# Kernel tuning notes

Hardware: AMD Instinct MI355X
Metric: run time of the kernel (lower is better)

Reference implementation:

```python
import jax, jax.numpy as jnp
from jax import lax
import numpy as np

PN_FEAT = 64


def _conv(x, w, b):
    # x: [B,H,W,Cin], w: [kh,kw,Cin,Cout] (SAME padding, stride 1)
    return lax.conv_general_dilated(x, w, (1, 1), 'SAME',
                                    dimension_numbers=('NHWC', 'HWIO', 'NHWC')) + b


def setup_inputs() -> dict:
    key = jax.random.key(0)
    ks = jax.random.split(key, 12)
    B, P, N, C = 4, 5000, 100, 8
    nx = ny = 240
    pillars = jax.random.normal(ks[0], (B, P, N, C), dtype=jnp.float32)
    pillar_idxs = jax.random.randint(ks[1], (B, P, 2), 0, nx).astype(jnp.int32)
    def lin(k, fi, fo):
        return jax.random.normal(k, (fi, fo), dtype=jnp.float32) / np.sqrt(fi).astype(np.float32)
    def cnv(k, kh, kw, ci, co):
        return jax.random.normal(k, (kh, kw, ci, co), dtype=jnp.float32) / np.sqrt(kh * kw * ci).astype(np.float32)
    return {
        'pillars': pillars,
        'pillar_idxs': pillar_idxs,
        'nx': nx,
        'ny': ny,
        # pointnet MLP: 8 -> 64 (tanh) -> 64
        'pn_w0': lin(ks[2], 8, 64), 'pn_b0': jnp.zeros((64,), jnp.float32),
        'pn_w1': lin(ks[3], 64, PN_FEAT), 'pn_b1': jnp.zeros((PN_FEAT,), jnp.float32),
        # resnet costmap CNN: 64 -> 128 (tanh) -> 128 (tanh) -> 1, relu output
        'cw0': cnv(ks[4], 3, 3, PN_FEAT, 128), 'cb0': jnp.zeros((128,), jnp.float32),
        'cw1': cnv(ks[5], 3, 3, 128, 128), 'cb1': jnp.zeros((128,), jnp.float32),
        'cw2': cnv(ks[6], 1, 1, 128, 1), 'cb2': jnp.zeros((1,), jnp.float32),
    }


def reference(pillars, pillar_idxs, nx, ny,
              pn_w0, pn_b0, pn_w1, pn_b1,
              cw0, cb0, cw1, cb1, cw2, cb2):
    VALID_THRESH = 1000000.0
    ACT_SCALE = 1.0
    # mask padded points (norm >= 1e6 means invalid)
    valid = (jnp.linalg.norm(pillars, axis=-1, keepdims=True) < VALID_THRESH).astype(pillars.dtype)
    # per-point MLP: [B,P,N,8] -> [B,P,N,F]
    h = jnp.tanh(pillars @ pn_w0 + pn_b0)
    feat = h @ pn_w1 + pn_b1
    # masked max over points in each pillar -> [B,P,F]
    pmax = jnp.max(feat * valid, axis=-2)
    # scatter pillar features into BEV pseudo-image [B,nx,ny,F]
    B = pillars.shape[0]
    bidx = jnp.arange(B)[:, None]                      # [B,1]
    img = jnp.zeros((B, nx, ny, PN_FEAT), pillars.dtype)
    img = img.at[bidx, pillar_idxs[..., 0], pillar_idxs[..., 1]].set(pmax)
    # costmap CNN head (NHWC internally; original is NCHW, same math)
    x = jnp.tanh(_conv(img, cw0, cb0))
    x = jnp.tanh(_conv(x, cw1, cb1))
    x = _conv(x, cw2, cb2)
    return jax.nn.relu(x) * ACT_SCALE            # [B,nx,ny,1]
```

## Files before the change

kernel.cpp:

```cpp
#include <hip/hip_runtime.h>
#include <hip/hip_bf16.h>
#include <math.h>

#define B  4
#define P  5000
#define NPT 100
#define F  64
#define NX 240
#define NY 240
#define C1 128

typedef __attribute__((ext_vector_type(8)))  short short8;
typedef __attribute__((ext_vector_type(16))) float f32x16;

__device__ __forceinline__ float tanh_fast(float x) {
    float e = __expf(2.0f * x);
    float r = __builtin_amdgcn_rcpf(e + 1.0f);
    return __builtin_fmaf(-2.0f, r, 1.0f);
}
__device__ __forceinline__ short bf16_bits(float f) {
    return (short)(__bfloat16_as_ushort(__float2bfloat16(f)));
}

__global__ __launch_bounds__(128) void pn_mfma_kernel(
    const float* __restrict__ pillars,
    const short* __restrict__ w0p,
    const float* __restrict__ b0,
    const __hip_bfloat16* __restrict__ w1t,
    const float* __restrict__ b1,
    float* __restrict__ pmax)
{
    constexpr int HS = F + 8;
    constexpr int XS = 40;
    __shared__ short xA[128 * XS];
    __shared__ short hA[128 * HS];
    __shared__ float red[2][F];
    __shared__ unsigned int vb32[4];

    int bp = blockIdx.x;
    int n  = threadIdx.x;
    int wave = n >> 6, lane = n & 63;
    int mr = lane & 31;
    int g  = lane >> 5;
    bool live = (n < NPT);

    const float* xp = pillars + ((size_t)bp * NPT + (live ? n : 0)) * 8;
    float4 q0 = *(const float4*)xp;
    float4 q1 = *(const float4*)(xp + 4);
    float x[8] = {q0.x, q0.y, q0.z, q0.w, q1.x, q1.y, q1.z, q1.w};

    float ss = 0.f;
#pragma unroll
    for (int c = 0; c < 8; c++) ss += x[c] * x[c];
    bool valid = live && (ss < 1e12f);

    unsigned long long bal = __ballot(valid);
    if (lane == 0) {
        vb32[wave * 2]     = (unsigned)bal;
        vb32[wave * 2 + 1] = (unsigned)(bal >> 32);
    }

    short8 xhi, xlo, xz;
#pragma unroll
    for (int c = 0; c < 8; c++) {
        __hip_bfloat16 hb = __float2bfloat16(x[c]);
        float hv = __bfloat162float(hb);
        xhi[c] = (short)__bfloat16_as_ushort(hb);
        xlo[c] = bf16_bits(x[c] - hv);
        xz[c] = 0;
    }
    *(short8*)&xA[n * XS + 0]  = xhi;
    *(short8*)&xA[n * XS + 8]  = xlo;
    *(short8*)&xA[n * XS + 16] = xhi;
    *(short8*)&xA[n * XS + 24] = xz;
    __syncthreads();

    short8 wb[2][2];
#pragma unroll
    for (int kk = 0; kk < 2; kk++)
#pragma unroll
        for (int nt = 0; nt < 2; nt++)
            wb[kk][nt] = *(const short8*)(w0p + ((kk * 2 + g) * 64 + nt * 32 + mr) * 8);

    f32x16 hc00 = {0,0,0,0,0,0,0,0,0,0,0,0,0,0,0,0};
    f32x16 hc01 = hc00, hc10 = hc00, hc11 = hc00;
#pragma unroll
    for (int kk = 0; kk < 2; kk++) {
        short8 a0 = *(const short8*)&xA[(wave * 64 + mr) * XS + kk * 16 + g * 8];
        short8 a1 = *(const short8*)&xA[(wave * 64 + 32 + mr) * XS + kk * 16 + g * 8];
        hc00 = __builtin_amdgcn_mfma_f32_32x32x16_bf16(a0, wb[kk][0], hc00, 0, 0, 0);
        hc01 = __builtin_amdgcn_mfma_f32_32x32x16_bf16(a0, wb[kk][1], hc01, 0, 0, 0);
        hc10 = __builtin_amdgcn_mfma_f32_32x32x16_bf16(a1, wb[kk][0], hc10, 0, 0, 0);
        hc11 = __builtin_amdgcn_mfma_f32_32x32x16_bf16(a1, wb[kk][1], hc11, 0, 0, 0);
    }

    float b00 = b0[mr];
    float b01 = b0[32 + mr];
#pragma unroll
    for (int mt = 0; mt < 2; mt++) {
#pragma unroll
        for (int r = 0; r < 16; r++) {
            int prow = wave * 64 + mt * 32 + (r & 3) + 8 * (r >> 2) + 4 * g;
            float h0 = (mt == 0) ? hc00[r] : hc10[r];
            float h1 = (mt == 0) ? hc01[r] : hc11[r];
            hA[prow * HS + mr]      = bf16_bits(tanh_fast(h0 + b00));
            hA[prow * HS + 32 + mr] = bf16_bits(tanh_fast(h1 + b01));
        }
    }
    __syncthreads();

    short8 bfrag[2][4];
#pragma unroll
    for (int nt = 0; nt < 2; nt++)
#pragma unroll
        for (int c0 = 0; c0 < 4; c0++)
            bfrag[nt][c0] = *(const short8*)((const short*)w1t +
                                (nt * 32 + mr) * F + c0 * 16 + g * 8);

    f32x16 acc00 = {0,0,0,0,0,0,0,0,0,0,0,0,0,0,0,0};
    f32x16 acc01 = acc00, acc10 = acc00, acc11 = acc00;

    const short* arow = &hA[(wave * 64 + mr) * HS + g * 8];
#pragma unroll
    for (int c0 = 0; c0 < 4; c0++) {
        short8 af0 = *(const short8*)(arow + c0 * 16);
        short8 af1 = *(const short8*)(arow + 32 * HS + c0 * 16);
        acc00 = __builtin_amdgcn_mfma_f32_32x32x16_bf16(af0, bfrag[0][c0], acc00, 0, 0, 0);
        acc01 = __builtin_amdgcn_mfma_f32_32x32x16_bf16(af0, bfrag[1][c0], acc01, 0, 0, 0);
        acc10 = __builtin_amdgcn_mfma_f32_32x32x16_bf16(af1, bfrag[0][c0], acc10, 0, 0, 0);
        acc11 = __builtin_amdgcn_mfma_f32_32x32x16_bf16(af1, bfrag[1][c0], acc11, 0, 0, 0);
    }

    float bv0 = b1[mr];
    float bv1 = b1[32 + mr];
    bool allv = ((vb32[0] & vb32[1] & vb32[2]) == 0xFFFFFFFFu) &&
                ((vb32[3] & 0xFu) == 0xFu);
    float mx0 = -INFINITY, mx1 = -INFINITY;

    if (allv) {
#pragma unroll
        for (int mt = 0; mt < 2; mt++) {
#pragma unroll
            for (int r = 0; r < 16; r++) {
                bool inc = !(wave == 1 && mt == 1) || (g == 0 && r < 4);
                if (inc) {
                    mx0 = fmaxf(mx0, (mt == 0) ? acc00[r] : acc10[r]);
                    mx1 = fmaxf(mx1, (mt == 0) ? acc01[r] : acc11[r]);
                }
            }
        }
        mx0 += bv0;
        mx1 += bv1;
    } else {
        unsigned wm0 = vb32[wave * 2];
        unsigned wm1 = vb32[wave * 2 + 1];
#pragma unroll
        for (int mt = 0; mt < 2; mt++) {
            unsigned wm = (mt == 0) ? wm0 : wm1;
#pragma unroll
            for (int r = 0; r < 16; r++) {
                int idx = (r & 3) + 8 * (r >> 2) + 4 * g;
                bool inc = !(wave == 1 && mt == 1) || (idx < 4);
                if (inc) {
                    bool vbit = (wm >> idx) & 1;
                    float a0 = (mt == 0) ? acc00[r] : acc10[r];
                    float a1 = (mt == 0) ? acc01[r] : acc11[r];
                    mx0 = fmaxf(mx0, vbit ? (a0 + bv0) : 0.0f);
                    mx1 = fmaxf(mx1, vbit ? (a1 + bv1) : 0.0f);
                }
            }
        }
    }
    mx0 = fmaxf(mx0, __shfl_xor(mx0, 32, 64));
    mx1 = fmaxf(mx1, __shfl_xor(mx1, 32, 64));
    if (lane < 32) { red[wave][mr] = mx0; red[wave][32 + mr] = mx1; }
    __syncthreads();
    if (n < F)
        pmax[(size_t)bp * F + n] = fmaxf(red[0][n], red[1][n]);
}

__global__ __launch_bounds__(256) void winner_kernel(
    const int* __restrict__ idxs, int* __restrict__ winner)
{
    int i = blockIdx.x * 256 + threadIdx.x;
    if (i >= B * P) return;
    int ix = idxs[i * 2], iy = idxs[i * 2 + 1];
    int b = i / P, p = i % P;
    atomicMax(&winner[(b * NX + ix) * NY + iy], p);
}

__global__ __launch_bounds__(64) void scatter_kernel(
    const int* __restrict__ idxs, const int* __restrict__ winner,
    const float* __restrict__ pmax, __hip_bfloat16* __restrict__ img)
{
    int bp = blockIdx.x;
    int f = threadIdx.x;
    int ix = idxs[bp * 2], iy = idxs[bp * 2 + 1];
    int b = bp / P, p = bp % P;
    int cell = (b * NX + ix) * NY + iy;
    if (winner[cell] == p)
        img[(size_t)cell * F + f] = __float2bfloat16(pmax[(size_t)bp * F + f]);
}

__global__ __launch_bounds__(256) void cvt_w_kernel(
    const float* __restrict__ w, __hip_bfloat16* __restrict__ wt, int cin)
{
    int idx = blockIdx.x * 256 + threadIdx.x;
    int total = 9 * cin * 128;
    if (idx >= total) return;
    int co = idx % 128;
    int rest = idx / 128;
    int ci = rest % cin;
    int t  = rest / cin;
    int c0 = ci >> 4, c16 = ci & 15;
    wt[(((size_t)(t * (cin >> 4) + c0)) * 128 + co) * 16 + c16] = __float2bfloat16(w[idx]);
}

__global__ __launch_bounds__(256) void cvt_w1_kernel(
    const float* __restrict__ w1, __hip_bfloat16* __restrict__ w1t)
{
    int idx = blockIdx.x * 256 + threadIdx.x;
    if (idx >= F * F) return;
    int k = idx >> 6, nn = idx & 63;
    w1t[nn * F + k] = __float2bfloat16(w1[idx]);
}

__global__ __launch_bounds__(256) void cvt_w0p_kernel(
    const float* __restrict__ w0, short* __restrict__ w0p)
{
    int idx = blockIdx.x * 256 + threadIdx.x;
    if (idx >= 4 * 64 * 8) return;
    int j = idx & 7;
    int nn = (idx >> 3) & 63;
    int s = idx >> 9;
    float wv = w0[j * F + nn];
    __hip_bfloat16 hb = __float2bfloat16(wv);
    short out = 0;
    if (s < 2)      out = (short)__bfloat16_as_ushort(hb);
    else if (s == 2) out = bf16_bits(wv - __bfloat162float(hb));
    w0p[idx] = out;
}

template<int CIN, bool FUSE>
__global__ __launch_bounds__(256, 3) void conv_mfma(
    const __hip_bfloat16* __restrict__ in,
    const __hip_bfloat16* __restrict__ wt,
    const float* __restrict__ bias,
    const float* __restrict__ w2,
    const float* __restrict__ b2,
    __hip_bfloat16* __restrict__ out_bf,
    float* __restrict__ out_f)
{
    constexpr int PASSES = CIN / 64;
    constexpr int CI   = 64;
    constexpr int NC16 = CI / 16;
    constexpr int ROWS = 4 * 98;
    __shared__ short sP[ROWS * 64];
    __shared__ float sred[FUSE ? 2 : 1][2][96];

    int tid  = threadIdx.x;
    int wave = tid >> 6;
    int lane = tid & 63;
    int mr = lane & 31;
    int g  = lane >> 5;
    int coh = wave & 1;
    int xr  = wave >> 1;
    int x0 = blockIdx.x * 2;
    int y0 = blockIdx.y * 72;
    int b  = blockIdx.z;
    int n0 = coh * 64;

    const short* wts = (const short*)wt;

    f32x16 acc[3][2];
#pragma unroll
    for (int mt = 0; mt < 3; mt++)
#pragma unroll
        for (int nt = 0; nt < 2; nt++)
            acc[mt][nt] = (f32x16){0,0,0,0,0,0,0,0,0,0,0,0,0,0,0,0};

#pragma unroll
    for (int p = 0; p < PASSES; p++) {
        if (p) __syncthreads();

        for (int i = 0; i < 13; i++) {
            int t = tid + i * 256;
            if (t < ROWS * 8) {
                int c8  = t & 7;
                int row = t >> 3;
                int dx = row / 98, dy = row - dx * 98;
                int gx = x0 - 1 + dx, gy = y0 - 1 + dy;
                float4 v = make_float4(0.f, 0.f, 0.f, 0.f);
                if (gx >= 0 && gx < NX && gy >= 0 && gy < NY)
                    v = *(const float4*)&in[(((size_t)b * NX + gx) * NY + gy) * CIN + p * CI + c8 * 8];
                *(float4*)&sP[row * 64 + ((c8 ^ (row & 7)) * 8)] = v;
            }
        }
        __syncthreads();

#pragma unroll
        for (int tap = 0; tap < 9; tap++) {
            int kh = tap / 3, kw = tap % 3;
            int rowbase = (xr + kh) * 98 + kw + mr;
            int r7 = rowbase & 7;
            const short* abase = sP + rowbase * 64;
            const short* wrow = wts + ((size_t)(tap * (CIN / 16) + p * NC16) * 128 + n0 + mr) * 16 + g * 8;
#pragma unroll
            for (int c0 = 0; c0 < NC16; c0++) {
                short8 w0f = *(const short8*)(wrow + (size_t)c0 * 2048);
                short8 w1f = *(const short8*)(wrow + (size_t)c0 * 2048 + 512);
                int goff = ((c0 * 2 + g) ^ r7) * 8;
                short8 a0 = *(const short8*)(abase + goff);
                short8 a1 = *(const short8*)(abase + 32 * 64 + goff);
                short8 a2 = *(const short8*)(abase + 64 * 64 + goff);
                acc[0][0] = __builtin_amdgcn_mfma_f32_32x32x16_bf16(a0, w0f, acc[0][0], 0, 0, 0);
                acc[0][1] = __builtin_amdgcn_mfma_f32_32x32x16_bf16(a0, w1f, acc[0][1], 0, 0, 0);
                acc[1][0] = __builtin_amdgcn_mfma_f32_32x32x16_bf16(a1, w0f, acc[1][0], 0, 0, 0);
                acc[1][1] = __builtin_amdgcn_mfma_f32_32x32x16_bf16(a1, w1f, acc[1][1], 0, 0, 0);
                acc[2][0] = __builtin_amdgcn_mfma_f32_32x32x16_bf16(a2, w0f, acc[2][0], 0, 0, 0);
                acc[2][1] = __builtin_amdgcn_mfma_f32_32x32x16_bf16(a2, w1f, acc[2][1], 0, 0, 0);
            }
        }
    }

    float bv0 = bias[n0 + mr];
    float bv1 = bias[n0 + 32 + mr];
    if (!FUSE) {
        size_t base = ((size_t)b * NX + (x0 + xr)) * NY;
#pragma unroll
        for (int mt = 0; mt < 3; mt++) {
#pragma unroll
            for (int r = 0; r < 16; r++) {
                int y = y0 + mt * 32 + (r & 3) + 8 * (r >> 2) + 4 * g;
                out_bf[(base + y) * C1 + n0 + mr]      = __float2bfloat16(tanh_fast(acc[mt][0][r] + bv0));
                out_bf[(base + y) * C1 + n0 + 32 + mr] = __float2bfloat16(tanh_fast(acc[mt][1][r] + bv1));
            }
        }
    } else {
        float w20 = w2[n0 + mr];
        float w21 = w2[n0 + 32 + mr];
#pragma unroll
        for (int mt = 0; mt < 3; mt++) {
#pragma unroll
            for (int r = 0; r < 16; r++) {
                float v = tanh_fast(acc[mt][0][r] + bv0) * w20
                        + tanh_fast(acc[mt][1][r] + bv1) * w21;
                v += __shfl_xor(v, 1, 64);
                v += __shfl_xor(v, 2, 64);
                v += __shfl_xor(v, 4, 64);
                v += __shfl_xor(v, 8, 64);
                v += __shfl_xor(v, 16, 64);
                if (mr == 0)
                    sred[coh][xr][mt * 32 + (r & 3) + 8 * (r >> 2) + 4 * g] = v;
            }
        }
        __syncthreads();
        if (tid < 192) {
            int xr2 = tid / 96;
            int yy  = tid % 96;
            float r = sred[0][xr2][yy] + sred[1][xr2][yy] + b2[0];
            out_f[((size_t)b * NX + (x0 + xr2)) * NY + (y0 + yy)] = fmaxf(r, 0.f);
        }
    }
}

extern "C" void kernel_launch(void* const* d_in, const int* in_sizes, int n_in,
                              void* d_out, int out_size, void* d_ws, size_t ws_size,
                              hipStream_t stream) {
    const float* pillars = (const float*)d_in[0];
    const int*   idxs    = (const int*)d_in[1];
    const float* pn_w0   = (const float*)d_in[4];
    const float* pn_b0   = (const float*)d_in[5];
    const float* pn_w1   = (const float*)d_in[6];
    const float* pn_b1   = (const float*)d_in[7];
    const float* cw0     = (const float*)d_in[8];
    const float* cb0     = (const float*)d_in[9];
    const float* cw1     = (const float*)d_in[10];
    const float* cb1     = (const float*)d_in[11];
    const float* cw2     = (const float*)d_in[12];
    const float* cb2     = (const float*)d_in[13];
    float* out = (float*)d_out;

    char* ws = (char*)d_ws;
    const size_t IMG_BYTES  = (size_t)B * NX * NY * F * 2;
    const size_t OUT1_BYTES = (size_t)B * NX * NY * C1 * 2;
    const size_t WIN_BYTES  = (size_t)B * NX * NY * 4;
    const size_t PMAX_BYTES = (size_t)B * P * F * 4;
    const size_t WT1_BYTES  = (size_t)9 * C1 * F * 2;
    const size_t WT2_BYTES  = (size_t)9 * C1 * C1 * 2;
    const size_t W1T_BYTES  = (size_t)F * F * 2;
    __hip_bfloat16* img  = (__hip_bfloat16*)ws;
    __hip_bfloat16* out1 = (__hip_bfloat16*)(ws + IMG_BYTES);
    int*   winner = (int*)(ws + IMG_BYTES + OUT1_BYTES);
    float* pmax   = (float*)(ws + IMG_BYTES + OUT1_BYTES + WIN_BYTES);
    __hip_bfloat16* wt1 = (__hip_bfloat16*)(ws + IMG_BYTES + OUT1_BYTES + WIN_BYTES + PMAX_BYTES);
    __hip_bfloat16* wt2 = (__hip_bfloat16*)(ws + IMG_BYTES + OUT1_BYTES + WIN_BYTES + PMAX_BYTES + WT1_BYTES);
    __hip_bfloat16* w1t = (__hip_bfloat16*)(ws + IMG_BYTES + OUT1_BYTES + WIN_BYTES + PMAX_BYTES + WT1_BYTES + WT2_BYTES);
    short* w0p = (short*)(ws + IMG_BYTES + OUT1_BYTES + WIN_BYTES + PMAX_BYTES + WT1_BYTES + WT2_BYTES + W1T_BYTES);

    hipMemsetAsync(img, 0, IMG_BYTES, stream);
    hipMemsetAsync(winner, 0xFF, WIN_BYTES, stream);

    cvt_w_kernel<<<(9 * F * C1 + 255) / 256, 256, 0, stream>>>(cw0, wt1, F);
    cvt_w_kernel<<<(9 * C1 * C1 + 255) / 256, 256, 0, stream>>>(cw1, wt2, C1);
    cvt_w1_kernel<<<(F * F + 255) / 256, 256, 0, stream>>>(pn_w1, w1t);
    cvt_w0p_kernel<<<(4 * 64 * 8 + 255) / 256, 256, 0, stream>>>(pn_w0, w0p);

    pn_mfma_kernel<<<B * P, 128, 0, stream>>>(pillars, w0p, pn_b0, w1t, pn_b1, pmax);
    winner_kernel<<<(B * P + 255) / 256, 256, 0, stream>>>(idxs, winner);
    scatter_kernel<<<B * P, 64, 0, stream>>>(idxs, winner, pmax, img);

    conv_mfma<F, false><<<dim3(NX / 2, 3, B), 256, 0, stream>>>(
        img, wt1, cb0, nullptr, nullptr, out1, nullptr);
    conv_mfma<C1, true><<<dim3(NX / 2, 3, B), 256, 0, stream>>>(
        out1, wt2, cb1, cw2, cb2, nullptr, out);
}
```

Baseline: 386.7 us.

## Stage conv input tiles with async global-to-LDS loads and smaller row tiles

```diff
diff --git a/kernel.cpp b/kernel.cpp
--- a/kernel.cpp
+++ b/kernel.cpp
@@ -20,6 +20,11 @@
 }
 __device__ __forceinline__ short bf16_bits(float f) {
     return (short)(__bfloat16_as_ushort(__float2bfloat16(f)));
+}
+__device__ __forceinline__ void async_load16(const void* g, void* l) {
+    __builtin_amdgcn_global_load_lds(
+        (const __attribute__((address_space(1))) void*)g,
+        (__attribute__((address_space(3))) void*)l, 16, 0, 0);
 }
 
 __global__ __launch_bounds__(128) void pn_mfma_kernel(
@@ -248,15 +253,16 @@
     const float* __restrict__ bias,
     const float* __restrict__ w2,
     const float* __restrict__ b2,
+    const __hip_bfloat16* __restrict__ zerobuf,
     __hip_bfloat16* __restrict__ out_bf,
     float* __restrict__ out_f)
 {
     constexpr int PASSES = CIN / 64;
     constexpr int CI   = 64;
     constexpr int NC16 = CI / 16;
-    constexpr int ROWS = 4 * 98;
-    __shared__ short sP[ROWS * 64];
-    __shared__ float sred[FUSE ? 2 : 1][2][96];
+    constexpr int CSTR = 272;
+    __shared__ short sP[8 * CSTR * 8];
+    __shared__ float sred[FUSE ? 2 : 1][2][64];
 
     int tid  = threadIdx.x;
     int wave = tid >> 6;
@@ -266,15 +272,16 @@
     int coh = wave & 1;
     int xr  = wave >> 1;
     int x0 = blockIdx.x * 2;
-    int y0 = blockIdx.y * 72;
+    int y0 = blockIdx.y * 62;
+    if (y0 > 178) y0 = 178;
     int b  = blockIdx.z;
     int n0 = coh * 64;
 
     const short* wts = (const short*)wt;
 
-    f32x16 acc[3][2];
-#pragma unroll
-    for (int mt = 0; mt < 3; mt++)
+    f32x16 acc[2][2];
+#pragma unroll
+    for (int mt = 0; mt < 2; mt++)
 #pragma unroll
         for (int nt = 0; nt < 2; nt++)
             acc[mt][nt] = (f32x16){0,0,0,0,0,0,0,0,0,0,0,0,0,0,0,0};
@@ -283,17 +290,20 @@
     for (int p = 0; p < PASSES; p++) {
         if (p) __syncthreads();
 
-        for (int i = 0; i < 13; i++) {
-            int t = tid + i * 256;
-            if (t < ROWS * 8) {
-                int c8  = t & 7;
-                int row = t >> 3;
-                int dx = row / 98, dy = row - dx * 98;
-                int gx = x0 - 1 + dx, gy = y0 - 1 + dy;
-                float4 v = make_float4(0.f, 0.f, 0.f, 0.f);
-                if (gx >= 0 && gx < NX && gy >= 0 && gy < NY)
-                    v = *(const float4*)&in[(((size_t)b * NX + gx) * NY + gy) * CIN + p * CI + c8 * 8];
-                *(float4*)&sP[row * 64 + ((c8 ^ (row & 7)) * 8)] = v;
+        {
+            int gy = y0 - 1 + lane;
+            bool yok = (gy >= 0 && gy < NY);
+#pragma unroll
+            for (int j = 0; j < 8; j++) {
+                int q  = j * 4 + wave;
+                int cc = q >> 2;
+                int dx = q & 3;
+                int gx = x0 - 1 + dx;
+                const __hip_bfloat16* src =
+                    (yok && gx >= 0 && gx < NX)
+                    ? &in[(((size_t)b * NX + gx) * NY + gy) * CIN + p * CI + cc * 8]
+                    : zerobuf;
+                async_load16(src, (void*)(sP + (cc * CSTR + dx * 64) * 8));
             }
         }
         __syncthreads();
@@ -301,24 +311,20 @@
 #pragma unroll
         for (int tap = 0; tap < 9; tap++) {
             int kh = tap / 3, kw = tap % 3;
-            int rowbase = (xr + kh) * 98 + kw + mr;
-            int r7 = rowbase & 7;
-            const short* abase = sP + rowbase * 64;
+            int rowcol = (xr + kh) * 64 + kw;
             const short* wrow = wts + ((size_t)(tap * (CIN / 16) + p * NC16) * 128 + n0 + mr) * 16 + g * 8;
 #pragma unroll
             for (int c0 = 0; c0 < NC16; c0++) {
                 short8 w0f = *(const short8*)(wrow + (size_t)c0 * 2048);
                 short8 w1f = *(const short8*)(wrow + (size_t)c0 * 2048 + 512);
-                int goff = ((c0 * 2 + g) ^ r7) * 8;
-                short8 a0 = *(const short8*)(abase + goff);
-                short8 a1 = *(const short8*)(abase + 32 * 64 + goff);
-                short8 a2 = *(const short8*)(abase + 64 * 64 + goff);
+                int cc = c0 * 2 + g;
+                const short* abase = sP + (cc * CSTR + rowcol + mr) * 8;
+                short8 a0 = *(const short8*)(abase);
+                short8 a1 = *(const short8*)(abase + 32 * 8);
                 acc[0][0] = __builtin_amdgcn_mfma_f32_32x32x16_bf16(a0, w0f, acc[0][0], 0, 0, 0);
                 acc[0][1] = __builtin_amdgcn_mfma_f32_32x32x16_bf16(a0, w1f, acc[0][1], 0, 0, 0);
                 acc[1][0] = __builtin_amdgcn_mfma_f32_32x32x16_bf16(a1, w0f, acc[1][0], 0, 0, 0);
                 acc[1][1] = __builtin_amdgcn_mfma_f32_32x32x16_bf16(a1, w1f, acc[1][1], 0, 0, 0);
-                acc[2][0] = __builtin_amdgcn_mfma_f32_32x32x16_bf16(a2, w0f, acc[2][0], 0, 0, 0);
-                acc[2][1] = __builtin_amdgcn_mfma_f32_32x32x16_bf16(a2, w1f, acc[2][1], 0, 0, 0);
             }
         }
     }
@@ -328,19 +334,22 @@
     if (!FUSE) {
         size_t base = ((size_t)b * NX + (x0 + xr)) * NY;
 #pragma unroll
-        for (int mt = 0; mt < 3; mt++) {
+        for (int mt = 0; mt < 2; mt++) {
 #pragma unroll
             for (int r = 0; r < 16; r++) {
-                int y = y0 + mt * 32 + (r & 3) + 8 * (r >> 2) + 4 * g;
-                out_bf[(base + y) * C1 + n0 + mr]      = __float2bfloat16(tanh_fast(acc[mt][0][r] + bv0));
-                out_bf[(base + y) * C1 + n0 + 32 + mr] = __float2bfloat16(tanh_fast(acc[mt][1][r] + bv1));
+                int row = mt * 32 + (r & 3) + 8 * (r >> 2) + 4 * g;
+                if (row < 62) {
+                    int y = y0 + row;
+                    out_bf[(base + y) * C1 + n0 + mr]      = __float2bfloat16(tanh_fast(acc[mt][0][r] + bv0));
+                    out_bf[(base + y) * C1 + n0 + 32 + mr] = __float2bfloat16(tanh_fast(acc[mt][1][r] + bv1));
+                }
             }
         }
     } else {
         float w20 = w2[n0 + mr];
         float w21 = w2[n0 + 32 + mr];
 #pragma unroll
-        for (int mt = 0; mt < 3; mt++) {
+        for (int mt = 0; mt < 2; mt++) {
 #pragma unroll
             for (int r = 0; r < 16; r++) {
                 float v = tanh_fast(acc[mt][0][r] + bv0) * w20
@@ -355,11 +364,13 @@
             }
         }
         __syncthreads();
-        if (tid < 192) {
-            int xr2 = tid / 96;
-            int yy  = tid % 96;
-            float r = sred[0][xr2][yy] + sred[1][xr2][yy] + b2[0];
-            out_f[((size_t)b * NX + (x0 + xr2)) * NY + (y0 + yy)] = fmaxf(r, 0.f);
+        if (tid < 128) {
+            int xr2 = tid >> 6;
+            int yy  = tid & 63;
+            if (yy < 62) {
+                float r = sred[0][xr2][yy] + sred[1][xr2][yy] + b2[0];
+                out_f[((size_t)b * NX + (x0 + xr2)) * NY + (y0 + yy)] = fmaxf(r, 0.f);
+            }
         }
     }
 }
@@ -389,6 +400,7 @@
     const size_t WT1_BYTES  = (size_t)9 * C1 * F * 2;
     const size_t WT2_BYTES  = (size_t)9 * C1 * C1 * 2;
     const size_t W1T_BYTES  = (size_t)F * F * 2;
+    const size_t W0P_BYTES  = (size_t)4 * 64 * 8 * 2;
     __hip_bfloat16* img  = (__hip_bfloat16*)ws;
     __hip_bfloat16* out1 = (__hip_bfloat16*)(ws + IMG_BYTES);
     int*   winner = (int*)(ws + IMG_BYTES + OUT1_BYTES);
@@ -397,9 +409,11 @@
     __hip_bfloat16* wt2 = (__hip_bfloat16*)(ws + IMG_BYTES + OUT1_BYTES + WIN_BYTES + PMAX_BYTES + WT1_BYTES);
     __hip_bfloat16* w1t = (__hip_bfloat16*)(ws + IMG_BYTES + OUT1_BYTES + WIN_BYTES + PMAX_BYTES + WT1_BYTES + WT2_BYTES);
     short* w0p = (short*)(ws + IMG_BYTES + OUT1_BYTES + WIN_BYTES + PMAX_BYTES + WT1_BYTES + WT2_BYTES + W1T_BYTES);
+    __hip_bfloat16* zerobuf = (__hip_bfloat16*)(ws + IMG_BYTES + OUT1_BYTES + WIN_BYTES + PMAX_BYTES + WT1_BYTES + WT2_BYTES + W1T_BYTES + W0P_BYTES);
 
     hipMemsetAsync(img, 0, IMG_BYTES, stream);
     hipMemsetAsync(winner, 0xFF, WIN_BYTES, stream);
+    hipMemsetAsync(zerobuf, 0, 64, stream);
 
     cvt_w_kernel<<<(9 * F * C1 + 255) / 256, 256, 0, stream>>>(cw0, wt1, F);
     cvt_w_kernel<<<(9 * C1 * C1 + 255) / 256, 256, 0, stream>>>(cw1, wt2, C1);
@@ -410,8 +424,8 @@
     winner_kernel<<<(B * P + 255) / 256, 256, 0, stream>>>(idxs, winner);
     scatter_kernel<<<B * P, 64, 0, stream>>>(idxs, winner, pmax, img);
 
-    conv_mfma<F, false><<<dim3(NX / 2, 3, B), 256, 0, stream>>>(
-        img, wt1, cb0, nullptr, nullptr, out1, nullptr);
-    conv_mfma<C1, true><<<dim3(NX / 2, 3, B), 256, 0, stream>>>(
-        out1, wt2, cb1, cw2, cb2, nullptr, out);
-}
+    conv_mfma<F, false><<<dim3(NX / 2, 4, B), 256, 0, stream>>>(
+        img, wt1, cb0, nullptr, nullptr, zerobuf, out1, nullptr);
+    conv_mfma<C1, true><<<dim3(NX / 2, 4, B), 256, 0, stream>>>(
+        out1, wt2, cb1, cw2, cb2, zerobuf, nullptr, out);
+}
```

After: 357.9 us. 1.08x faster.
